# Kernel tuning notes

Measured on AMD Instinct MI355X. Metric: run time of the kernel, lower is better.

The kernel has to match this reference:

```python
import jax, jax.numpy as jnp
import numpy as np

N_PILLARS_X = 512
N_PILLARS_Y = 512
IN_FEATURES = 6
OUT_FEATURES = 64
N_POINTS = 2_000_000
BN_EPS = 1e-5


def setup_inputs() -> dict:
    key = jax.random.key(0)
    k_x, k_idx, k_w, k_b, k_g, k_bt = jax.random.split(key, 6)
    x = jax.random.normal(k_x, (N_POINTS, IN_FEATURES), dtype=jnp.float32)
    indices = jax.random.randint(k_idx, (N_POINTS, 2), 0, N_PILLARS_X, dtype=jnp.int64)
    # Linear params (torch default init scale ~ 1/sqrt(fan_in))
    bound = 1.0 / np.sqrt(IN_FEATURES)
    W = jax.random.uniform(k_w, (OUT_FEATURES, IN_FEATURES), minval=-bound, maxval=bound, dtype=jnp.float32)
    b = jax.random.uniform(k_b, (OUT_FEATURES,), minval=-bound, maxval=bound, dtype=jnp.float32)
    # BatchNorm affine params (torch init: gamma=1, beta=0; perturb gamma slightly)
    gamma = jnp.ones((OUT_FEATURES,), dtype=jnp.float32)
    beta = jnp.zeros((OUT_FEATURES,), dtype=jnp.float32)
    return {"x": x, "indices": indices, "W": W, "b": b, "gamma": gamma, "beta": beta}


def reference(x, indices, W, b, gamma, beta):
    # Linear: (N, 6) @ (6, 64) + b -> (N, 64)
    h = x @ W.T + b
    # BatchNorm1d (training mode: batch statistics, biased variance)
    mean = jnp.mean(h, axis=0)
    var = jnp.mean(jnp.square(h - mean), axis=0)
    h = gamma * (h - mean) * jax.lax.rsqrt(var + BN_EPS) + beta
    h = jax.nn.relu(h)
    # Scatter-add each point's feature vector into its (x_idx, y_idx) pillar cell
    grid = jnp.zeros((N_PILLARS_X, N_PILLARS_Y, OUT_FEATURES), dtype=h.dtype)
    grid = grid.at[indices[:, 0], indices[:, 1]].add(h)
    return grid
```

## Files before the change

### kernel.cpp

```cpp
#include <hip/hip_runtime.h>
#include <hip/hip_fp16.h>


constexpr int NPTS   = 2000000;
constexpr int NBUCK  = 2048;
constexpr int CPB    = 128;
constexpr int NBLK   = 256;
constexpr int CHUNK  = 7813;
constexpr float EPS  = 1e-5f;

constexpr int WS_WPH    = 0;
constexpr int WS_BP     = 192;
constexpr int WS_STARTS = 256;
constexpr int WS_HIST   = 2560;
constexpr int WS_BASES  = WS_HIST + NBLK * NBUCK;
constexpr int WS_BSTATS = WS_BASES + NBLK * NBUCK;
constexpr int WS_SORTED = WS_BSTATS + NBLK * 32;

typedef _Float16 h2v __attribute__((ext_vector_type(2)));

__device__ __forceinline__ float dot2u(unsigned int a, unsigned int b, float c) {
    union { unsigned int u; h2v h; } ca, cb;
    ca.u = a; cb.u = b;
    return __builtin_amdgcn_fdot2(ca.h, cb.h, c, false);
}

__device__ __forceinline__ float wave_sum64(float v) {
#pragma unroll
    for (int off = 32; off > 0; off >>= 1) v += __shfl_down(v, off, 64);
    return v;
}

__global__ __launch_bounds__(1024) void hist_kernel(const int2* __restrict__ idx,
                                                    int* __restrict__ hist) {
    __shared__ int lh[NBUCK];
    for (int i = threadIdx.x; i < NBUCK; i += 1024) lh[i] = 0;
    __syncthreads();
    const int beg = blockIdx.x * CHUNK;
    const int end = min(NPTS, beg + CHUNK);
    for (int p = beg + threadIdx.x; p < end; p += 1024) {
        const int2 ij = idx[p];
        atomicAdd(&lh[(ij.x << 2) | (ij.y >> 7)], 1);
    }
    __syncthreads();
    int* out = hist + blockIdx.x * NBUCK;
    for (int i = threadIdx.x; i < NBUCK; i += 1024) out[i] = lh[i];
}

__global__ __launch_bounds__(64) void colscan_kernel(const int* __restrict__ hist,
                                                     int* __restrict__ bases,
                                                     int* __restrict__ starts) {
    const int b = blockIdx.x * 64 + threadIdx.x;
    int run = 0;
    for (int blk = 0; blk < NBLK; ++blk) {
        bases[blk * NBUCK + b] = run;
        run += hist[blk * NBUCK + b];
    }
    starts[b] = run;
}

__global__ __launch_bounds__(1024) void scan_kernel(int* __restrict__ starts) {
    __shared__ int wsum[16];
    const int t = threadIdx.x, lane = t & 63, wv = t >> 6;
    const int v0 = starts[2 * t], v1 = starts[2 * t + 1];
    const int v = v0 + v1;
    int incl = v;
#pragma unroll
    for (int d = 1; d < 64; d <<= 1) {
        int u = __shfl_up(incl, d, 64);
        if (lane >= d) incl += u;
    }
    if (lane == 63) wsum[wv] = incl;
    __syncthreads();
    int pre = 0;
#pragma unroll
    for (int w = 0; w < 16; ++w) {
        int sv = wsum[w];
        if (w < wv) pre += sv;
    }
    const int excl = pre + incl - v;
    starts[2 * t] = excl;
    starts[2 * t + 1] = excl + v0;
    if (t == 1023) starts[NBUCK] = excl + v;
}

__global__ __launch_bounds__(1024) void scatter_kernel(const float* __restrict__ x,
                                                       const int2* __restrict__ idx,
                                                       const int* __restrict__ starts,
                                                       const int* __restrict__ bases,
                                                       uint4* __restrict__ sorted4,
                                                       float* __restrict__ bstats) {
    __shared__ int lbase[NBUCK];
    __shared__ int lcur[NBUCK];
    __shared__ float lstats[16][27];
    const int blk = blockIdx.x;
    for (int i = threadIdx.x; i < NBUCK; i += 1024) {
        lbase[i] = starts[i] + bases[blk * NBUCK + i];
        lcur[i] = 0;
    }
    __syncthreads();

    float acc[27];
#pragma unroll
    for (int i = 0; i < 27; ++i) acc[i] = 0.f;

    const int beg = blk * CHUNK;
    const int end = min(NPTS, beg + CHUNK);
    for (int p = beg + threadIdx.x; p < end; p += 1024) {
        const int2 ij = idx[p];
        const float2* xp = (const float2*)(x + (size_t)p * 6);
        const float2 a = xp[0], bq = xp[1], cq = xp[2];
        float v[6] = {a.x, a.y, bq.x, bq.y, cq.x, cq.y};
        int c = 6;
#pragma unroll
        for (int k = 0; k < 6; ++k) {
            acc[k] += v[k];
#pragma unroll
            for (int l = k; l < 6; ++l) { acc[c] += v[k] * v[l]; ++c; }
        }
        __half2 h0 = __floats2half2_rn(a.x, a.y);
        __half2 h1 = __floats2half2_rn(bq.x, bq.y);
        __half2 h2 = __floats2half2_rn(cq.x, cq.y);
        const int b = (ij.x << 2) | (ij.y >> 7);
        const int rank = atomicAdd(&lcur[b], 1);
        uint4 r;
        r.x = *(const unsigned int*)&h0;
        r.y = *(const unsigned int*)&h1;
        r.z = *(const unsigned int*)&h2;
        r.w = (unsigned int)(ij.y & 127);
        sorted4[lbase[b] + rank] = r;
    }

    const int lane = threadIdx.x & 63, wv = threadIdx.x >> 6;
#pragma unroll
    for (int i = 0; i < 27; ++i) {
        const float s = wave_sum64(acc[i]);
        if (lane == 0) lstats[wv][i] = s;
    }
    __syncthreads();
    if (threadIdx.x < 27) {
        float s = 0.f;
        for (int w = 0; w < 16; ++w) s += lstats[w][threadIdx.x];
        bstats[blk * 32 + threadIdx.x] = s;
    }
}

__global__ __launch_bounds__(64) void bnfold_kernel(const float* __restrict__ bstats,
                                                    const float* __restrict__ W,
                                                    const float* __restrict__ b,
                                                    const float* __restrict__ gamma,
                                                    const float* __restrict__ beta,
                                                    float* __restrict__ ws) {
    __shared__ float s27[27];
    __shared__ float m[6], C[36];
    const int t = threadIdx.x;
    if (t < 27) {
        float s = 0.f;
        for (int blk = 0; blk < NBLK; ++blk) s += bstats[blk * 32 + t];
        s27[t] = s;
    }
    __syncthreads();
    if (t == 0) {
        const float invN = 1.0f / (float)NPTS;
        float mm[6];
        for (int k = 0; k < 6; ++k) { mm[k] = s27[k] * invN; m[k] = mm[k]; }
        int c = 6;
        for (int k = 0; k < 6; ++k)
            for (int l = k; l < 6; ++l) {
                const float cov = s27[c] * invN - mm[k] * mm[l];
                ++c;
                C[k * 6 + l] = cov;
                C[l * 6 + k] = cov;
            }
    }
    __syncthreads();
    float w[6];
#pragma unroll
    for (int k = 0; k < 6; ++k) w[k] = W[t * 6 + k];
    float mh = b[t];
#pragma unroll
    for (int k = 0; k < 6; ++k) mh += w[k] * m[k];
    float var = 0.f;
#pragma unroll
    for (int k = 0; k < 6; ++k)
#pragma unroll
        for (int l = 0; l < 6; ++l) var += w[k] * w[l] * C[k * 6 + l];
    const float s = gamma[t] * rsqrtf(var + EPS);
    float wp[6];
#pragma unroll
    for (int k = 0; k < 6; ++k) wp[k] = w[k] * s;
    unsigned int* wsu = (unsigned int*)ws;
    __half2 p0 = __floats2half2_rn(wp[0], wp[1]);
    __half2 p1 = __floats2half2_rn(wp[2], wp[3]);
    __half2 p2 = __floats2half2_rn(wp[4], wp[5]);
    wsu[WS_WPH + t * 3 + 0] = *(const unsigned int*)&p0;
    wsu[WS_WPH + t * 3 + 1] = *(const unsigned int*)&p1;
    wsu[WS_WPH + t * 3 + 2] = *(const unsigned int*)&p2;
    ws[WS_BP + t] = beta[t] + s * (b[t] - mh);
}

constexpr int CAP = 1152;
constexpr int ACCT = 256;
constexpr int RPT  = (CAP + ACCT - 1) / ACCT;

__global__ __launch_bounds__(ACCT, 8) void accum_kernel(const uint4* __restrict__ sorted4,
                                                        const int* __restrict__ starts,
                                                        const float* __restrict__ wsf,
                                                        float* __restrict__ grid) {
    __shared__ uint4 recs[CAP];
    __shared__ int lhist[CPB];
    __shared__ int cstart[CPB + 1];
    const int t = threadIdx.x, lane = t & 63, wv = t >> 6;

    const int s = starts[blockIdx.x];
    const int e = starts[blockIdx.x + 1];
    const int n = min(e - s, CAP);

    for (int i = t; i < CPB; i += ACCT) lhist[i] = 0;

    const unsigned int* wsu = (const unsigned int*)wsf;
    const unsigned int wp0 = wsu[WS_WPH + lane * 3 + 0];
    const unsigned int wp1 = wsu[WS_WPH + lane * 3 + 1];
    const unsigned int wp2 = wsu[WS_WPH + lane * 3 + 2];
    const float bb = wsf[WS_BP + lane];
    __syncthreads();

    uint4 rr[RPT];
    int rkk[RPT];
#pragma unroll
    for (int u = 0; u < RPT; ++u) {
        const int i = t + u * ACCT;
        rkk[u] = -1;
        if (i < n) {
            rr[u] = sorted4[s + i];
            rkk[u] = atomicAdd(&lhist[(int)rr[u].w], 1);
        }
    }
    __syncthreads();

    if (wv == 0) {
        const int v0 = lhist[2 * lane], v1 = lhist[2 * lane + 1];
        const int v = v0 + v1;
        int incl = v;
#pragma unroll
        for (int d = 1; d < 64; d <<= 1) {
            int u = __shfl_up(incl, d, 64);
            if (lane >= d) incl += u;
        }
        const int excl = incl - v;
        cstart[2 * lane] = excl;
        cstart[2 * lane + 1] = excl + v0;
        if (lane == 63) cstart[CPB] = incl;
    }
    __syncthreads();

#pragma unroll
    for (int u = 0; u < RPT; ++u)
        if (rkk[u] >= 0) recs[cstart[(int)rr[u].w] + rkk[u]] = rr[u];
    __syncthreads();

    float* gbase = grid + (size_t)blockIdx.x * (CPB * 64);
    for (int c = wv; c < CPB; c += 4) {
        const int cs = __builtin_amdgcn_readfirstlane(cstart[c]);
        const int ce = __builtin_amdgcn_readfirstlane(cstart[c + 1]);
        float acc0 = 0.f, acc1 = 0.f;
        int p = cs;
        for (; p + 1 < ce; p += 2) {
            const uint4 ra = recs[p];
            const uint4 rb = recs[p + 1];
            const float h0 = dot2u(ra.x, wp0, dot2u(ra.y, wp1, dot2u(ra.z, wp2, bb)));
            const float h1 = dot2u(rb.x, wp0, dot2u(rb.y, wp1, dot2u(rb.z, wp2, bb)));
            acc0 += fmaxf(h0, 0.f);
            acc1 += fmaxf(h1, 0.f);
        }
        if (p < ce) {
            const uint4 ra = recs[p];
            acc0 += fmaxf(dot2u(ra.x, wp0, dot2u(ra.y, wp1, dot2u(ra.z, wp2, bb))), 0.f);
        }
        gbase[c * 64 + lane] = acc0 + acc1;
    }

    if (e - s > CAP) {
        __syncthreads();
        for (int base = s + CAP + wv * 64; base < e; base += 4 * 64) {
            const int m = min(64, e - base);
            uint4 rec = make_uint4(0u, 0u, 0u, 0u);
            if (lane < m) rec = sorted4[base + lane];
            for (int pt = 0; pt < m; ++pt) {
                const unsigned int c  = __builtin_amdgcn_readlane(rec.w, pt);
                const unsigned int x0 = __builtin_amdgcn_readlane(rec.x, pt);
                const unsigned int x1 = __builtin_amdgcn_readlane(rec.y, pt);
                const unsigned int x2 = __builtin_amdgcn_readlane(rec.z, pt);
                const float h = dot2u(x0, wp0, dot2u(x1, wp1, dot2u(x2, wp2, bb)));
                unsafeAtomicAdd(&gbase[c * 64 + lane], fmaxf(h, 0.f));
            }
        }
    }
}

extern "C" void kernel_launch(void* const* d_in, const int* in_sizes, int n_in,
                              void* d_out, int out_size, void* d_ws, size_t ws_size,
                              hipStream_t stream) {
    const float* x       = (const float*)d_in[0];
    const int2*  indices = (const int2*)d_in[1];
    const float* W       = (const float*)d_in[2];
    const float* b       = (const float*)d_in[3];
    const float* gamma   = (const float*)d_in[4];
    const float* beta    = (const float*)d_in[5];
    float* out = (float*)d_out;
    float* wsf = (float*)d_ws;
    int*   wsi = (int*)d_ws;

    int*   hist    = wsi + WS_HIST;
    int*   bases   = wsi + WS_BASES;
    int*   starts  = wsi + WS_STARTS;
    uint4* sorted4 = (uint4*)(wsi + WS_SORTED);
    float* bstats  = wsf + WS_BSTATS;

    hist_kernel<<<NBLK, 1024, 0, stream>>>(indices, hist);
    colscan_kernel<<<NBUCK / 64, 64, 0, stream>>>(hist, bases, starts);
    scan_kernel<<<1, 1024, 0, stream>>>(starts);
    scatter_kernel<<<NBLK, 1024, 0, stream>>>(x, indices, starts, bases, sorted4, bstats);
    bnfold_kernel<<<1, 64, 0, stream>>>(bstats, W, b, gamma, beta, wsf);
    accum_kernel<<<NBUCK, ACCT, 0, stream>>>(sorted4, starts, wsf, out);
}
```

Measured before the change: 229.6 us.

## Parallelize column scan into segmented passes with 16-bit histograms and double blocks

```diff
diff --git a/kernel.cpp b/kernel.cpp
--- a/kernel.cpp
+++ b/kernel.cpp
@@ -5,17 +5,21 @@
 constexpr int NPTS   = 2000000;
 constexpr int NBUCK  = 2048;
 constexpr int CPB    = 128;
-constexpr int NBLK   = 256;
-constexpr int CHUNK  = 7813;
+constexpr int NBLK   = 512;
+constexpr int CHUNK  = (NPTS + NBLK - 1) / NBLK;
+constexpr int NSEG   = 8;
+constexpr int SEGLEN = NBLK / NSEG;
 constexpr float EPS  = 1e-5f;
 
 constexpr int WS_WPH    = 0;
 constexpr int WS_BP     = 192;
 constexpr int WS_STARTS = 256;
-constexpr int WS_HIST   = 2560;
-constexpr int WS_BASES  = WS_HIST + NBLK * NBUCK;
-constexpr int WS_BSTATS = WS_BASES + NBLK * NBUCK;
-constexpr int WS_SORTED = WS_BSTATS + NBLK * 32;
+constexpr int WS_SEGT   = 2560;
+constexpr int WS_SEGB   = WS_SEGT + NSEG * NBUCK;
+constexpr int WS_BSTATS = WS_SEGB + NSEG * NBUCK;
+constexpr int WS_HIST16 = WS_BSTATS + NBLK * 32;
+constexpr int WS_BASE16 = WS_HIST16 + NBLK * NBUCK / 2;
+constexpr int WS_SORTED = WS_BASE16 + NBLK * NBUCK / 2;
 
 typedef _Float16 h2v __attribute__((ext_vector_type(2)));
 
@@ -32,7 +36,7 @@
 }
 
 __global__ __launch_bounds__(1024) void hist_kernel(const int2* __restrict__ idx,
-                                                    int* __restrict__ hist) {
+                                                    unsigned int* __restrict__ hist16) {
     __shared__ int lh[NBUCK];
     for (int i = threadIdx.x; i < NBUCK; i += 1024) lh[i] = 0;
     __syncthreads();
@@ -43,20 +47,32 @@
         atomicAdd(&lh[(ij.x << 2) | (ij.y >> 7)], 1);
     }
     __syncthreads();
-    int* out = hist + blockIdx.x * NBUCK;
-    for (int i = threadIdx.x; i < NBUCK; i += 1024) out[i] = lh[i];
-}
-
-__global__ __launch_bounds__(64) void colscan_kernel(const int* __restrict__ hist,
-                                                     int* __restrict__ bases,
-                                                     int* __restrict__ starts) {
-    const int b = blockIdx.x * 64 + threadIdx.x;
+    unsigned int* out = hist16 + blockIdx.x * (NBUCK / 2);
+    for (int i = threadIdx.x; i < NBUCK / 2; i += 1024)
+        out[i] = (unsigned int)lh[2 * i] | ((unsigned int)lh[2 * i + 1] << 16);
+}
+
+__global__ __launch_bounds__(256) void colscan_a(const unsigned short* __restrict__ hist16,
+                                                 int* __restrict__ segtot) {
+    const int gid = blockIdx.x * 256 + threadIdx.x;
+    const int col = gid & (NBUCK - 1), seg = gid >> 11;
+    int s = 0;
+#pragma unroll 8
+    for (int j = 0; j < SEGLEN; ++j) s += hist16[(seg * SEGLEN + j) * NBUCK + col];
+    segtot[seg * NBUCK + col] = s;
+}
+
+__global__ __launch_bounds__(256) void colscan_b(const int* __restrict__ segtot,
+                                                 int* __restrict__ segbase,
+                                                 int* __restrict__ starts) {
+    const int col = blockIdx.x * 256 + threadIdx.x;
     int run = 0;
-    for (int blk = 0; blk < NBLK; ++blk) {
-        bases[blk * NBUCK + b] = run;
-        run += hist[blk * NBUCK + b];
-    }
-    starts[b] = run;
+#pragma unroll
+    for (int sgi = 0; sgi < NSEG; ++sgi) {
+        segbase[sgi * NBUCK + col] = run;
+        run += segtot[sgi * NBUCK + col];
+    }
+    starts[col] = run;
 }
 
 __global__ __launch_bounds__(1024) void scan_kernel(int* __restrict__ starts) {
@@ -84,10 +100,24 @@
     if (t == 1023) starts[NBUCK] = excl + v;
 }
 
+__global__ __launch_bounds__(256) void colscan_c(const unsigned short* __restrict__ hist16,
+                                                 const int* __restrict__ segbase,
+                                                 unsigned short* __restrict__ bases16) {
+    const int gid = blockIdx.x * 256 + threadIdx.x;
+    const int col = gid & (NBUCK - 1), seg = gid >> 11;
+    int run = segbase[seg * NBUCK + col];
+#pragma unroll 8
+    for (int j = 0; j < SEGLEN; ++j) {
+        const int blk = seg * SEGLEN + j;
+        bases16[blk * NBUCK + col] = (unsigned short)run;
+        run += hist16[blk * NBUCK + col];
+    }
+}
+
 __global__ __launch_bounds__(1024) void scatter_kernel(const float* __restrict__ x,
                                                        const int2* __restrict__ idx,
                                                        const int* __restrict__ starts,
-                                                       const int* __restrict__ bases,
+                                                       const unsigned short* __restrict__ bases16,
                                                        uint4* __restrict__ sorted4,
                                                        float* __restrict__ bstats) {
     __shared__ int lbase[NBUCK];
@@ -95,7 +125,7 @@
     __shared__ float lstats[16][27];
     const int blk = blockIdx.x;
     for (int i = threadIdx.x; i < NBUCK; i += 1024) {
-        lbase[i] = starts[i] + bases[blk * NBUCK + i];
+        lbase[i] = starts[i] + (int)bases16[blk * NBUCK + i];
         lcur[i] = 0;
     }
     __syncthreads();
@@ -138,25 +168,36 @@
         if (lane == 0) lstats[wv][i] = s;
     }
     __syncthreads();
-    if (threadIdx.x < 27) {
+    if (threadIdx.x < 32) {
         float s = 0.f;
-        for (int w = 0; w < 16; ++w) s += lstats[w][threadIdx.x];
+        if (threadIdx.x < 27)
+            for (int w = 0; w < 16; ++w) s += lstats[w][threadIdx.x];
         bstats[blk * 32 + threadIdx.x] = s;
     }
 }
 
-__global__ __launch_bounds__(64) void bnfold_kernel(const float* __restrict__ bstats,
-                                                    const float* __restrict__ W,
-                                                    const float* __restrict__ b,
-                                                    const float* __restrict__ gamma,
-                                                    const float* __restrict__ beta,
-                                                    float* __restrict__ ws) {
+__global__ __launch_bounds__(1024) void bnfold_kernel(const float* __restrict__ bstats,
+                                                      const float* __restrict__ W,
+                                                      const float* __restrict__ b,
+                                                      const float* __restrict__ gamma,
+                                                      const float* __restrict__ beta,
+                                                      float* __restrict__ ws) {
+    __shared__ float lred[32][33];
     __shared__ float s27[27];
     __shared__ float m[6], C[36];
     const int t = threadIdx.x;
+    {
+        const int s = t & 31, seg = t >> 5;
+        float a = 0.f;
+#pragma unroll 4
+        for (int j = 0; j < NBLK / 32; ++j) a += bstats[(seg * (NBLK / 32) + j) * 32 + s];
+        lred[seg][s] = a;
+    }
+    __syncthreads();
     if (t < 27) {
         float s = 0.f;
-        for (int blk = 0; blk < NBLK; ++blk) s += bstats[blk * 32 + t];
+#pragma unroll
+        for (int g = 0; g < 32; ++g) s += lred[g][t];
         s27[t] = s;
     }
     __syncthreads();
@@ -174,29 +215,31 @@
             }
     }
     __syncthreads();
-    float w[6];
-#pragma unroll
-    for (int k = 0; k < 6; ++k) w[k] = W[t * 6 + k];
-    float mh = b[t];
-#pragma unroll
-    for (int k = 0; k < 6; ++k) mh += w[k] * m[k];
-    float var = 0.f;
-#pragma unroll
-    for (int k = 0; k < 6; ++k)
-#pragma unroll
-        for (int l = 0; l < 6; ++l) var += w[k] * w[l] * C[k * 6 + l];
-    const float s = gamma[t] * rsqrtf(var + EPS);
-    float wp[6];
-#pragma unroll
-    for (int k = 0; k < 6; ++k) wp[k] = w[k] * s;
-    unsigned int* wsu = (unsigned int*)ws;
-    __half2 p0 = __floats2half2_rn(wp[0], wp[1]);
-    __half2 p1 = __floats2half2_rn(wp[2], wp[3]);
-    __half2 p2 = __floats2half2_rn(wp[4], wp[5]);
-    wsu[WS_WPH + t * 3 + 0] = *(const unsigned int*)&p0;
-    wsu[WS_WPH + t * 3 + 1] = *(const unsigned int*)&p1;
-    wsu[WS_WPH + t * 3 + 2] = *(const unsigned int*)&p2;
-    ws[WS_BP + t] = beta[t] + s * (b[t] - mh);
+    if (t < 64) {
+        float w[6];
+#pragma unroll
+        for (int k = 0; k < 6; ++k) w[k] = W[t * 6 + k];
+        float mh = b[t];
+#pragma unroll
+        for (int k = 0; k < 6; ++k) mh += w[k] * m[k];
+        float var = 0.f;
+#pragma unroll
+        for (int k = 0; k < 6; ++k)
+#pragma unroll
+            for (int l = 0; l < 6; ++l) var += w[k] * w[l] * C[k * 6 + l];
+        const float s = gamma[t] * rsqrtf(var + EPS);
+        float wp[6];
+#pragma unroll
+        for (int k = 0; k < 6; ++k) wp[k] = w[k] * s;
+        unsigned int* wsu = (unsigned int*)ws;
+        __half2 p0 = __floats2half2_rn(wp[0], wp[1]);
+        __half2 p1 = __floats2half2_rn(wp[2], wp[3]);
+        __half2 p2 = __floats2half2_rn(wp[4], wp[5]);
+        wsu[WS_WPH + t * 3 + 0] = *(const unsigned int*)&p0;
+        wsu[WS_WPH + t * 3 + 1] = *(const unsigned int*)&p1;
+        wsu[WS_WPH + t * 3 + 2] = *(const unsigned int*)&p2;
+        ws[WS_BP + t] = beta[t] + s * (b[t] - mh);
+    }
 }
 
 constexpr int CAP = 1152;
@@ -311,16 +354,21 @@
     float* wsf = (float*)d_ws;
     int*   wsi = (int*)d_ws;
 
-    int*   hist    = wsi + WS_HIST;
-    int*   bases   = wsi + WS_BASES;
+    unsigned int*   hist16u = (unsigned int*)(wsi + WS_HIST16);
+    unsigned short* hist16  = (unsigned short*)(wsi + WS_HIST16);
+    unsigned short* bases16 = (unsigned short*)(wsi + WS_BASE16);
+    int*   segtot  = wsi + WS_SEGT;
+    int*   segbase = wsi + WS_SEGB;
     int*   starts  = wsi + WS_STARTS;
     uint4* sorted4 = (uint4*)(wsi + WS_SORTED);
     float* bstats  = wsf + WS_BSTATS;
 
-    hist_kernel<<<NBLK, 1024, 0, stream>>>(indices, hist);
-    colscan_kernel<<<NBUCK / 64, 64, 0, stream>>>(hist, bases, starts);
+    hist_kernel<<<NBLK, 1024, 0, stream>>>(indices, hist16u);
+    colscan_a<<<NSEG * NBUCK / 256, 256, 0, stream>>>(hist16, segtot);
+    colscan_b<<<NBUCK / 256, 256, 0, stream>>>(segtot, segbase, starts);
     scan_kernel<<<1, 1024, 0, stream>>>(starts);
-    scatter_kernel<<<NBLK, 1024, 0, stream>>>(x, indices, starts, bases, sorted4, bstats);
-    bnfold_kernel<<<1, 64, 0, stream>>>(bstats, W, b, gamma, beta, wsf);
+    colscan_c<<<NSEG * NBUCK / 256, 256, 0, stream>>>(hist16, segbase, bases16);
+    scatter_kernel<<<NBLK, 1024, 0, stream>>>(x, indices, starts, bases16, sorted4, bstats);
+    bnfold_kernel<<<1, 1024, 0, stream>>>(bstats, W, b, gamma, beta, wsf);
     accum_kernel<<<NBUCK, ACCT, 0, stream>>>(sorted4, starts, wsf, out);
 }
```

New measurement: 216.9 us. -5.5%, faster.

## Replace histogram-scan sort with fixed-capacity bucket slots plus overflow list

Applied to the files above, without the earlier changes.

```diff
diff --git a/kernel.cpp b/kernel.cpp
--- a/kernel.cpp
+++ b/kernel.cpp
@@ -5,17 +5,22 @@
 constexpr int NPTS   = 2000000;
 constexpr int NBUCK  = 2048;
 constexpr int CPB    = 128;
-constexpr int NBLK   = 256;
-constexpr int CHUNK  = 7813;
+constexpr int NBLK   = 512;
+constexpr int CHUNK  = (NPTS + NBLK - 1) / NBLK;
 constexpr float EPS  = 1e-5f;
+
+constexpr int CAPR = 1148;
+constexpr int OCAP = 4096;
+constexpr int ACCT = 256;
+constexpr int RPT  = (CAPR + ACCT - 1) / ACCT;
 
 constexpr int WS_WPH    = 0;
 constexpr int WS_BP     = 192;
-constexpr int WS_STARTS = 256;
-constexpr int WS_HIST   = 2560;
-constexpr int WS_BASES  = WS_HIST + NBLK * NBUCK;
-constexpr int WS_BSTATS = WS_BASES + NBLK * NBUCK;
-constexpr int WS_SORTED = WS_BSTATS + NBLK * 32;
+constexpr int WS_BCUR   = 256;
+constexpr int WS_OCNT   = WS_BCUR + NBUCK * 16;
+constexpr int WS_BSTATS = WS_OCNT + 16;
+constexpr int WS_OLIST  = WS_BSTATS + NBLK * 32;
+constexpr int WS_SORTED = WS_OLIST + OCAP * 4;
 
 typedef _Float16 h2v __attribute__((ext_vector_type(2)));
 
@@ -31,74 +36,15 @@
     return v;
 }
 
-__global__ __launch_bounds__(1024) void hist_kernel(const int2* __restrict__ idx,
-                                                    int* __restrict__ hist) {
-    __shared__ int lh[NBUCK];
-    for (int i = threadIdx.x; i < NBUCK; i += 1024) lh[i] = 0;
-    __syncthreads();
-    const int beg = blockIdx.x * CHUNK;
-    const int end = min(NPTS, beg + CHUNK);
-    for (int p = beg + threadIdx.x; p < end; p += 1024) {
-        const int2 ij = idx[p];
-        atomicAdd(&lh[(ij.x << 2) | (ij.y >> 7)], 1);
-    }
-    __syncthreads();
-    int* out = hist + blockIdx.x * NBUCK;
-    for (int i = threadIdx.x; i < NBUCK; i += 1024) out[i] = lh[i];
-}
-
-__global__ __launch_bounds__(64) void colscan_kernel(const int* __restrict__ hist,
-                                                     int* __restrict__ bases,
-                                                     int* __restrict__ starts) {
-    const int b = blockIdx.x * 64 + threadIdx.x;
-    int run = 0;
-    for (int blk = 0; blk < NBLK; ++blk) {
-        bases[blk * NBUCK + b] = run;
-        run += hist[blk * NBUCK + b];
-    }
-    starts[b] = run;
-}
-
-__global__ __launch_bounds__(1024) void scan_kernel(int* __restrict__ starts) {
-    __shared__ int wsum[16];
-    const int t = threadIdx.x, lane = t & 63, wv = t >> 6;
-    const int v0 = starts[2 * t], v1 = starts[2 * t + 1];
-    const int v = v0 + v1;
-    int incl = v;
-#pragma unroll
-    for (int d = 1; d < 64; d <<= 1) {
-        int u = __shfl_up(incl, d, 64);
-        if (lane >= d) incl += u;
-    }
-    if (lane == 63) wsum[wv] = incl;
-    __syncthreads();
-    int pre = 0;
-#pragma unroll
-    for (int w = 0; w < 16; ++w) {
-        int sv = wsum[w];
-        if (w < wv) pre += sv;
-    }
-    const int excl = pre + incl - v;
-    starts[2 * t] = excl;
-    starts[2 * t + 1] = excl + v0;
-    if (t == 1023) starts[NBUCK] = excl + v;
-}
-
 __global__ __launch_bounds__(1024) void scatter_kernel(const float* __restrict__ x,
                                                        const int2* __restrict__ idx,
-                                                       const int* __restrict__ starts,
-                                                       const int* __restrict__ bases,
+                                                       int* __restrict__ wsi,
                                                        uint4* __restrict__ sorted4,
+                                                       uint4* __restrict__ olist,
                                                        float* __restrict__ bstats) {
-    __shared__ int lbase[NBUCK];
-    __shared__ int lcur[NBUCK];
     __shared__ float lstats[16][27];
+    int* bcur = wsi + WS_BCUR;
     const int blk = blockIdx.x;
-    for (int i = threadIdx.x; i < NBUCK; i += 1024) {
-        lbase[i] = starts[i] + bases[blk * NBUCK + i];
-        lcur[i] = 0;
-    }
-    __syncthreads();
 
     float acc[27];
 #pragma unroll
@@ -121,14 +67,20 @@
         __half2 h0 = __floats2half2_rn(a.x, a.y);
         __half2 h1 = __floats2half2_rn(bq.x, bq.y);
         __half2 h2 = __floats2half2_rn(cq.x, cq.y);
-        const int b = (ij.x << 2) | (ij.y >> 7);
-        const int rank = atomicAdd(&lcur[b], 1);
+        const int cell = (ij.x << 9) | ij.y;
+        const int bk = cell >> 7;
+        const int slot = atomicAdd(&bcur[bk * 16], 1);
         uint4 r;
         r.x = *(const unsigned int*)&h0;
         r.y = *(const unsigned int*)&h1;
         r.z = *(const unsigned int*)&h2;
-        r.w = (unsigned int)(ij.y & 127);
-        sorted4[lbase[b] + rank] = r;
+        if (slot < CAPR) {
+            r.w = (unsigned int)(cell & 127);
+            sorted4[(size_t)bk * CAPR + slot] = r;
+        } else {
+            const int os = atomicAdd(wsi + WS_OCNT, 1);
+            if (os < OCAP) { r.w = (unsigned int)cell; olist[os] = r; }
+        }
     }
 
     const int lane = threadIdx.x & 63, wv = threadIdx.x >> 6;
@@ -138,25 +90,36 @@
         if (lane == 0) lstats[wv][i] = s;
     }
     __syncthreads();
-    if (threadIdx.x < 27) {
+    if (threadIdx.x < 32) {
         float s = 0.f;
-        for (int w = 0; w < 16; ++w) s += lstats[w][threadIdx.x];
+        if (threadIdx.x < 27)
+            for (int w = 0; w < 16; ++w) s += lstats[w][threadIdx.x];
         bstats[blk * 32 + threadIdx.x] = s;
     }
 }
 
-__global__ __launch_bounds__(64) void bnfold_kernel(const float* __restrict__ bstats,
-                                                    const float* __restrict__ W,
-                                                    const float* __restrict__ b,
-                                                    const float* __restrict__ gamma,
-                                                    const float* __restrict__ beta,
-                                                    float* __restrict__ ws) {
+__global__ __launch_bounds__(1024) void bnfold_kernel(const float* __restrict__ bstats,
+                                                      const float* __restrict__ W,
+                                                      const float* __restrict__ b,
+                                                      const float* __restrict__ gamma,
+                                                      const float* __restrict__ beta,
+                                                      float* __restrict__ ws) {
+    __shared__ float lred[32][33];
     __shared__ float s27[27];
     __shared__ float m[6], C[36];
     const int t = threadIdx.x;
+    {
+        const int s = t & 31, seg = t >> 5;
+        float a = 0.f;
+#pragma unroll 4
+        for (int j = 0; j < NBLK / 32; ++j) a += bstats[(seg * (NBLK / 32) + j) * 32 + s];
+        lred[seg][s] = a;
+    }
+    __syncthreads();
     if (t < 27) {
         float s = 0.f;
-        for (int blk = 0; blk < NBLK; ++blk) s += bstats[blk * 32 + t];
+#pragma unroll
+        for (int g = 0; g < 32; ++g) s += lred[g][t];
         s27[t] = s;
     }
     __syncthreads();
@@ -174,47 +137,44 @@
             }
     }
     __syncthreads();
-    float w[6];
-#pragma unroll
-    for (int k = 0; k < 6; ++k) w[k] = W[t * 6 + k];
-    float mh = b[t];
-#pragma unroll
-    for (int k = 0; k < 6; ++k) mh += w[k] * m[k];
-    float var = 0.f;
-#pragma unroll
-    for (int k = 0; k < 6; ++k)
-#pragma unroll
-        for (int l = 0; l < 6; ++l) var += w[k] * w[l] * C[k * 6 + l];
-    const float s = gamma[t] * rsqrtf(var + EPS);
-    float wp[6];
-#pragma unroll
-    for (int k = 0; k < 6; ++k) wp[k] = w[k] * s;
-    unsigned int* wsu = (unsigned int*)ws;
-    __half2 p0 = __floats2half2_rn(wp[0], wp[1]);
-    __half2 p1 = __floats2half2_rn(wp[2], wp[3]);
-    __half2 p2 = __floats2half2_rn(wp[4], wp[5]);
-    wsu[WS_WPH + t * 3 + 0] = *(const unsigned int*)&p0;
-    wsu[WS_WPH + t * 3 + 1] = *(const unsigned int*)&p1;
-    wsu[WS_WPH + t * 3 + 2] = *(const unsigned int*)&p2;
-    ws[WS_BP + t] = beta[t] + s * (b[t] - mh);
-}
-
-constexpr int CAP = 1152;
-constexpr int ACCT = 256;
-constexpr int RPT  = (CAP + ACCT - 1) / ACCT;
+    if (t < 64) {
+        float w[6];
+#pragma unroll
+        for (int k = 0; k < 6; ++k) w[k] = W[t * 6 + k];
+        float mh = b[t];
+#pragma unroll
+        for (int k = 0; k < 6; ++k) mh += w[k] * m[k];
+        float var = 0.f;
+#pragma unroll
+        for (int k = 0; k < 6; ++k)
+#pragma unroll
+            for (int l = 0; l < 6; ++l) var += w[k] * w[l] * C[k * 6 + l];
+        const float s = gamma[t] * rsqrtf(var + EPS);
+        float wp[6];
+#pragma unroll
+        for (int k = 0; k < 6; ++k) wp[k] = w[k] * s;
+        unsigned int* wsu = (unsigned int*)ws;
+        __half2 p0 = __floats2half2_rn(wp[0], wp[1]);
+        __half2 p1 = __floats2half2_rn(wp[2], wp[3]);
+        __half2 p2 = __floats2half2_rn(wp[4], wp[5]);
+        wsu[WS_WPH + t * 3 + 0] = *(const unsigned int*)&p0;
+        wsu[WS_WPH + t * 3 + 1] = *(const unsigned int*)&p1;
+        wsu[WS_WPH + t * 3 + 2] = *(const unsigned int*)&p2;
+        ws[WS_BP + t] = beta[t] + s * (b[t] - mh);
+    }
+}
 
 __global__ __launch_bounds__(ACCT, 8) void accum_kernel(const uint4* __restrict__ sorted4,
-                                                        const int* __restrict__ starts,
+                                                        const int* __restrict__ wsi,
                                                         const float* __restrict__ wsf,
+                                                        const uint4* __restrict__ olist,
                                                         float* __restrict__ grid) {
-    __shared__ uint4 recs[CAP];
+    __shared__ uint4 recs[CAPR];
     __shared__ int lhist[CPB];
     __shared__ int cstart[CPB + 1];
     const int t = threadIdx.x, lane = t & 63, wv = t >> 6;
-
-    const int s = starts[blockIdx.x];
-    const int e = starts[blockIdx.x + 1];
-    const int n = min(e - s, CAP);
+    const int b = blockIdx.x;
+    const int n = min(wsi[WS_BCUR + b * 16], CAPR);
 
     for (int i = t; i < CPB; i += ACCT) lhist[i] = 0;
 
@@ -225,6 +185,7 @@
     const float bb = wsf[WS_BP + lane];
     __syncthreads();
 
+    const uint4* src = sorted4 + (size_t)b * CAPR;
     uint4 rr[RPT];
     int rkk[RPT];
 #pragma unroll
@@ -232,7 +193,7 @@
         const int i = t + u * ACCT;
         rkk[u] = -1;
         if (i < n) {
-            rr[u] = sorted4[s + i];
+            rr[u] = src[i];
             rkk[u] = atomicAdd(&lhist[(int)rr[u].w], 1);
         }
     }
@@ -259,40 +220,53 @@
         if (rkk[u] >= 0) recs[cstart[(int)rr[u].w] + rkk[u]] = rr[u];
     __syncthreads();
 
-    float* gbase = grid + (size_t)blockIdx.x * (CPB * 64);
-    for (int c = wv; c < CPB; c += 4) {
-        const int cs = __builtin_amdgcn_readfirstlane(cstart[c]);
-        const int ce = __builtin_amdgcn_readfirstlane(cstart[c + 1]);
-        float acc0 = 0.f, acc1 = 0.f;
-        int p = cs;
-        for (; p + 1 < ce; p += 2) {
-            const uint4 ra = recs[p];
-            const uint4 rb = recs[p + 1];
-            const float h0 = dot2u(ra.x, wp0, dot2u(ra.y, wp1, dot2u(ra.z, wp2, bb)));
-            const float h1 = dot2u(rb.x, wp0, dot2u(rb.y, wp1, dot2u(rb.z, wp2, bb)));
-            acc0 += fmaxf(h0, 0.f);
-            acc1 += fmaxf(h1, 0.f);
-        }
-        if (p < ce) {
-            const uint4 ra = recs[p];
-            acc0 += fmaxf(dot2u(ra.x, wp0, dot2u(ra.y, wp1, dot2u(ra.z, wp2, bb))), 0.f);
-        }
-        gbase[c * 64 + lane] = acc0 + acc1;
-    }
-
-    if (e - s > CAP) {
+    float* gbase = grid + (size_t)b * (CPB * 64);
+    const int c0 = wv * 32, climit = c0 + 32;
+    int c = c0;
+    int ce = __builtin_amdgcn_readfirstlane(cstart[c0 + 1]);
+    const int wbeg = __builtin_amdgcn_readfirstlane(cstart[c0]);
+    const int wend = __builtin_amdgcn_readfirstlane(cstart[climit]);
+    float acc = 0.f;
+
+    auto flush = [&](int pnext) {
+        while (c < climit && ce == pnext) {
+            gbase[c * 64 + lane] = acc;
+            acc = 0.f;
+            ++c;
+            if (c < climit) ce = __builtin_amdgcn_readfirstlane(cstart[c + 1]);
+        }
+    };
+    flush(wbeg);
+    int p = wbeg;
+    for (; p + 4 <= wend; p += 4) {
+        const uint4 r0 = recs[p];
+        const uint4 r1 = recs[p + 1];
+        const uint4 r2 = recs[p + 2];
+        const uint4 r3 = recs[p + 3];
+        const float h0 = dot2u(r0.x, wp0, dot2u(r0.y, wp1, dot2u(r0.z, wp2, bb)));
+        const float h1 = dot2u(r1.x, wp0, dot2u(r1.y, wp1, dot2u(r1.z, wp2, bb)));
+        const float h2 = dot2u(r2.x, wp0, dot2u(r2.y, wp1, dot2u(r2.z, wp2, bb)));
+        const float h3 = dot2u(r3.x, wp0, dot2u(r3.y, wp1, dot2u(r3.z, wp2, bb)));
+        acc += fmaxf(h0, 0.f); flush(p + 1);
+        acc += fmaxf(h1, 0.f); flush(p + 2);
+        acc += fmaxf(h2, 0.f); flush(p + 3);
+        acc += fmaxf(h3, 0.f); flush(p + 4);
+    }
+    for (; p < wend; ++p) {
+        const uint4 r0 = recs[p];
+        acc += fmaxf(dot2u(r0.x, wp0, dot2u(r0.y, wp1, dot2u(r0.z, wp2, bb))), 0.f);
+        flush(p + 1);
+    }
+
+    const int ocn = min(wsi[WS_OCNT], OCAP);
+    if (ocn > 0) {
         __syncthreads();
-        for (int base = s + CAP + wv * 64; base < e; base += 4 * 64) {
-            const int m = min(64, e - base);
-            uint4 rec = make_uint4(0u, 0u, 0u, 0u);
-            if (lane < m) rec = sorted4[base + lane];
-            for (int pt = 0; pt < m; ++pt) {
-                const unsigned int c  = __builtin_amdgcn_readlane(rec.w, pt);
-                const unsigned int x0 = __builtin_amdgcn_readlane(rec.x, pt);
-                const unsigned int x1 = __builtin_amdgcn_readlane(rec.y, pt);
-                const unsigned int x2 = __builtin_amdgcn_readlane(rec.z, pt);
-                const float h = dot2u(x0, wp0, dot2u(x1, wp1, dot2u(x2, wp2, bb)));
-                unsafeAtomicAdd(&gbase[c * 64 + lane], fmaxf(h, 0.f));
+        for (int i = wv; i < ocn; i += 4) {
+            const uint4 r = olist[i];
+            const int cell = (int)r.w;
+            if ((cell >> 7) == b) {
+                const float h = dot2u(r.x, wp0, dot2u(r.y, wp1, dot2u(r.z, wp2, bb)));
+                unsafeAtomicAdd(&gbase[(cell & 127) * 64 + lane], fmaxf(h, 0.f));
             }
         }
     }
@@ -311,16 +285,12 @@
     float* wsf = (float*)d_ws;
     int*   wsi = (int*)d_ws;
 
-    int*   hist    = wsi + WS_HIST;
-    int*   bases   = wsi + WS_BASES;
-    int*   starts  = wsi + WS_STARTS;
     uint4* sorted4 = (uint4*)(wsi + WS_SORTED);
+    uint4* olist   = (uint4*)(wsi + WS_OLIST);
     float* bstats  = wsf + WS_BSTATS;
 
-    hist_kernel<<<NBLK, 1024, 0, stream>>>(indices, hist);
-    colscan_kernel<<<NBUCK / 64, 64, 0, stream>>>(hist, bases, starts);
-    scan_kernel<<<1, 1024, 0, stream>>>(starts);
-    scatter_kernel<<<NBLK, 1024, 0, stream>>>(x, indices, starts, bases, sorted4, bstats);
-    bnfold_kernel<<<1, 64, 0, stream>>>(bstats, W, b, gamma, beta, wsf);
-    accum_kernel<<<NBUCK, ACCT, 0, stream>>>(sorted4, starts, wsf, out);
-}
+    hipMemsetAsync(wsi + WS_BCUR, 0, (size_t)(WS_BSTATS - WS_BCUR) * sizeof(int), stream);
+    scatter_kernel<<<NBLK, 1024, 0, stream>>>(x, indices, wsi, sorted4, olist, bstats);
+    bnfold_kernel<<<1, 1024, 0, stream>>>(bstats, W, b, gamma, beta, wsf);
+    accum_kernel<<<NBUCK, ACCT, 0, stream>>>(sorted4, wsi, wsf, olist, out);
+}
```

Measured after the change: 285.3 us. 24.2% more time.

## Fuse histogram, scan and scatter into block-local LDS sort with per-chunk regions

Applied to the files above, without the earlier changes.

```diff
diff --git a/kernel.cpp b/kernel.cpp
--- a/kernel.cpp
+++ b/kernel.cpp
@@ -5,17 +5,15 @@
 constexpr int NPTS   = 2000000;
 constexpr int NBUCK  = 2048;
 constexpr int CPB    = 128;
-constexpr int NBLK   = 256;
-constexpr int CHUNK  = 7813;
+constexpr int NBLK   = 512;
+constexpr int CHUNK  = (NPTS + NBLK - 1) / NBLK;
 constexpr float EPS  = 1e-5f;
 
 constexpr int WS_WPH    = 0;
 constexpr int WS_BP     = 192;
-constexpr int WS_STARTS = 256;
-constexpr int WS_HIST   = 2560;
-constexpr int WS_BASES  = WS_HIST + NBLK * NBUCK;
-constexpr int WS_BSTATS = WS_BASES + NBLK * NBUCK;
-constexpr int WS_SORTED = WS_BSTATS + NBLK * 32;
+constexpr int WS_BSTATS = 256;
+constexpr int WS_OFFT   = WS_BSTATS + NBLK * 32;
+constexpr int WS_REG    = WS_OFFT + (NBUCK + 1) * NBLK / 2;
 
 typedef _Float16 h2v __attribute__((ext_vector_type(2)));
 
@@ -31,82 +29,59 @@
     return v;
 }
 
-__global__ __launch_bounds__(1024) void hist_kernel(const int2* __restrict__ idx,
-                                                    int* __restrict__ hist) {
+__global__ __launch_bounds__(1024) void sort_kernel(const float* __restrict__ x,
+                                                    const int2* __restrict__ idx,
+                                                    unsigned short* __restrict__ offt,
+                                                    uint4* __restrict__ regions,
+                                                    float* __restrict__ bstats) {
+    __shared__ uint4 recs[CHUNK];
     __shared__ int lh[NBUCK];
-    for (int i = threadIdx.x; i < NBUCK; i += 1024) lh[i] = 0;
-    __syncthreads();
-    const int beg = blockIdx.x * CHUNK;
-    const int end = min(NPTS, beg + CHUNK);
-    for (int p = beg + threadIdx.x; p < end; p += 1024) {
+    __shared__ int wsum[16];
+    __shared__ float lstats[16][27];
+    const int t = threadIdx.x, lane = t & 63, wv = t >> 6;
+    const int blk = blockIdx.x;
+    const int ch  = ((blk & 7) << 6) | (blk >> 3);
+    const int beg = ch * CHUNK, end = min(NPTS, beg + CHUNK), cnt = end - beg;
+
+    for (int i = t; i < NBUCK; i += 1024) lh[i] = 0;
+    __syncthreads();
+
+    for (int p = beg + t; p < end; p += 1024) {
         const int2 ij = idx[p];
         atomicAdd(&lh[(ij.x << 2) | (ij.y >> 7)], 1);
     }
     __syncthreads();
-    int* out = hist + blockIdx.x * NBUCK;
-    for (int i = threadIdx.x; i < NBUCK; i += 1024) out[i] = lh[i];
-}
-
-__global__ __launch_bounds__(64) void colscan_kernel(const int* __restrict__ hist,
-                                                     int* __restrict__ bases,
-                                                     int* __restrict__ starts) {
-    const int b = blockIdx.x * 64 + threadIdx.x;
-    int run = 0;
-    for (int blk = 0; blk < NBLK; ++blk) {
-        bases[blk * NBUCK + b] = run;
-        run += hist[blk * NBUCK + b];
-    }
-    starts[b] = run;
-}
-
-__global__ __launch_bounds__(1024) void scan_kernel(int* __restrict__ starts) {
-    __shared__ int wsum[16];
-    const int t = threadIdx.x, lane = t & 63, wv = t >> 6;
-    const int v0 = starts[2 * t], v1 = starts[2 * t + 1];
-    const int v = v0 + v1;
-    int incl = v;
-#pragma unroll
-    for (int d = 1; d < 64; d <<= 1) {
-        int u = __shfl_up(incl, d, 64);
-        if (lane >= d) incl += u;
-    }
-    if (lane == 63) wsum[wv] = incl;
-    __syncthreads();
-    int pre = 0;
-#pragma unroll
-    for (int w = 0; w < 16; ++w) {
-        int sv = wsum[w];
-        if (w < wv) pre += sv;
-    }
-    const int excl = pre + incl - v;
-    starts[2 * t] = excl;
-    starts[2 * t + 1] = excl + v0;
-    if (t == 1023) starts[NBUCK] = excl + v;
-}
-
-__global__ __launch_bounds__(1024) void scatter_kernel(const float* __restrict__ x,
-                                                       const int2* __restrict__ idx,
-                                                       const int* __restrict__ starts,
-                                                       const int* __restrict__ bases,
-                                                       uint4* __restrict__ sorted4,
-                                                       float* __restrict__ bstats) {
-    __shared__ int lbase[NBUCK];
-    __shared__ int lcur[NBUCK];
-    __shared__ float lstats[16][27];
-    const int blk = blockIdx.x;
-    for (int i = threadIdx.x; i < NBUCK; i += 1024) {
-        lbase[i] = starts[i] + bases[blk * NBUCK + i];
-        lcur[i] = 0;
+
+    {
+        const int v0 = lh[2 * t], v1 = lh[2 * t + 1];
+        const int v = v0 + v1;
+        int incl = v;
+#pragma unroll
+        for (int d = 1; d < 64; d <<= 1) {
+            int u = __shfl_up(incl, d, 64);
+            if (lane >= d) incl += u;
+        }
+        if (lane == 63) wsum[wv] = incl;
+        __syncthreads();
+        int pre = 0;
+#pragma unroll
+        for (int w = 0; w < 16; ++w) {
+            int sv = wsum[w];
+            if (w < wv) pre += sv;
+        }
+        const int excl = pre + incl - v;
+        offt[(2 * t) * NBLK + ch]     = (unsigned short)excl;
+        offt[(2 * t + 1) * NBLK + ch] = (unsigned short)(excl + v0);
+        if (t == 1023) offt[NBUCK * NBLK + ch] = (unsigned short)(excl + v);
+        lh[2 * t] = excl;
+        lh[2 * t + 1] = excl + v0;
     }
     __syncthreads();
 
     float acc[27];
 #pragma unroll
     for (int i = 0; i < 27; ++i) acc[i] = 0.f;
-
-    const int beg = blk * CHUNK;
-    const int end = min(NPTS, beg + CHUNK);
-    for (int p = beg + threadIdx.x; p < end; p += 1024) {
+    for (int p = beg + t; p < end; p += 1024) {
         const int2 ij = idx[p];
         const float2* xp = (const float2*)(x + (size_t)p * 6);
         const float2 a = xp[0], bq = xp[1], cq = xp[2];
@@ -122,41 +97,55 @@
         __half2 h1 = __floats2half2_rn(bq.x, bq.y);
         __half2 h2 = __floats2half2_rn(cq.x, cq.y);
         const int b = (ij.x << 2) | (ij.y >> 7);
-        const int rank = atomicAdd(&lcur[b], 1);
+        const int dst = atomicAdd(&lh[b], 1);
         uint4 r;
         r.x = *(const unsigned int*)&h0;
         r.y = *(const unsigned int*)&h1;
         r.z = *(const unsigned int*)&h2;
         r.w = (unsigned int)(ij.y & 127);
-        sorted4[lbase[b] + rank] = r;
-    }
-
-    const int lane = threadIdx.x & 63, wv = threadIdx.x >> 6;
+        recs[dst] = r;
+    }
+    __syncthreads();
+
+    uint4* reg = regions + (size_t)ch * CHUNK;
+    for (int i = t; i < cnt; i += 1024) reg[i] = recs[i];
+
 #pragma unroll
     for (int i = 0; i < 27; ++i) {
         const float s = wave_sum64(acc[i]);
         if (lane == 0) lstats[wv][i] = s;
     }
     __syncthreads();
-    if (threadIdx.x < 27) {
+    if (t < 32) {
         float s = 0.f;
-        for (int w = 0; w < 16; ++w) s += lstats[w][threadIdx.x];
-        bstats[blk * 32 + threadIdx.x] = s;
-    }
-}
-
-__global__ __launch_bounds__(64) void bnfold_kernel(const float* __restrict__ bstats,
-                                                    const float* __restrict__ W,
-                                                    const float* __restrict__ b,
-                                                    const float* __restrict__ gamma,
-                                                    const float* __restrict__ beta,
-                                                    float* __restrict__ ws) {
+        if (t < 27)
+            for (int w = 0; w < 16; ++w) s += lstats[w][t];
+        bstats[ch * 32 + t] = s;
+    }
+}
+
+__global__ __launch_bounds__(1024) void bnfold_kernel(const float* __restrict__ bstats,
+                                                      const float* __restrict__ W,
+                                                      const float* __restrict__ b,
+                                                      const float* __restrict__ gamma,
+                                                      const float* __restrict__ beta,
+                                                      float* __restrict__ ws) {
+    __shared__ float lred[32][33];
     __shared__ float s27[27];
     __shared__ float m[6], C[36];
     const int t = threadIdx.x;
+    {
+        const int s = t & 31, seg = t >> 5;
+        float a = 0.f;
+#pragma unroll 4
+        for (int j = 0; j < NBLK / 32; ++j) a += bstats[(seg * (NBLK / 32) + j) * 32 + s];
+        lred[seg][s] = a;
+    }
+    __syncthreads();
     if (t < 27) {
         float s = 0.f;
-        for (int blk = 0; blk < NBLK; ++blk) s += bstats[blk * 32 + t];
+#pragma unroll
+        for (int g = 0; g < 32; ++g) s += lred[g][t];
         s27[t] = s;
     }
     __syncthreads();
@@ -174,66 +163,112 @@
             }
     }
     __syncthreads();
-    float w[6];
-#pragma unroll
-    for (int k = 0; k < 6; ++k) w[k] = W[t * 6 + k];
-    float mh = b[t];
-#pragma unroll
-    for (int k = 0; k < 6; ++k) mh += w[k] * m[k];
-    float var = 0.f;
-#pragma unroll
-    for (int k = 0; k < 6; ++k)
-#pragma unroll
-        for (int l = 0; l < 6; ++l) var += w[k] * w[l] * C[k * 6 + l];
-    const float s = gamma[t] * rsqrtf(var + EPS);
-    float wp[6];
-#pragma unroll
-    for (int k = 0; k < 6; ++k) wp[k] = w[k] * s;
-    unsigned int* wsu = (unsigned int*)ws;
-    __half2 p0 = __floats2half2_rn(wp[0], wp[1]);
-    __half2 p1 = __floats2half2_rn(wp[2], wp[3]);
-    __half2 p2 = __floats2half2_rn(wp[4], wp[5]);
-    wsu[WS_WPH + t * 3 + 0] = *(const unsigned int*)&p0;
-    wsu[WS_WPH + t * 3 + 1] = *(const unsigned int*)&p1;
-    wsu[WS_WPH + t * 3 + 2] = *(const unsigned int*)&p2;
-    ws[WS_BP + t] = beta[t] + s * (b[t] - mh);
-}
-
-constexpr int CAP = 1152;
-constexpr int ACCT = 256;
-constexpr int RPT  = (CAP + ACCT - 1) / ACCT;
-
-__global__ __launch_bounds__(ACCT, 8) void accum_kernel(const uint4* __restrict__ sorted4,
-                                                        const int* __restrict__ starts,
+    if (t < 64) {
+        float w[6];
+#pragma unroll
+        for (int k = 0; k < 6; ++k) w[k] = W[t * 6 + k];
+        float mh = b[t];
+#pragma unroll
+        for (int k = 0; k < 6; ++k) mh += w[k] * m[k];
+        float var = 0.f;
+#pragma unroll
+        for (int k = 0; k < 6; ++k)
+#pragma unroll
+            for (int l = 0; l < 6; ++l) var += w[k] * w[l] * C[k * 6 + l];
+        const float s = gamma[t] * rsqrtf(var + EPS);
+        float wp[6];
+#pragma unroll
+        for (int k = 0; k < 6; ++k) wp[k] = w[k] * s;
+        unsigned int* wsu = (unsigned int*)ws;
+        __half2 p0 = __floats2half2_rn(wp[0], wp[1]);
+        __half2 p1 = __floats2half2_rn(wp[2], wp[3]);
+        __half2 p2 = __floats2half2_rn(wp[4], wp[5]);
+        wsu[WS_WPH + t * 3 + 0] = *(const unsigned int*)&p0;
+        wsu[WS_WPH + t * 3 + 1] = *(const unsigned int*)&p1;
+        wsu[WS_WPH + t * 3 + 2] = *(const unsigned int*)&p2;
+        ws[WS_BP + t] = beta[t] + s * (b[t] - mh);
+    }
+}
+
+constexpr int CAP   = 1216;
+constexpr int OVCAP = 64;
+constexpr int ACCT  = 256;
+constexpr int RPT   = (CAP + ACCT - 1) / ACCT;
+
+__global__ __launch_bounds__(ACCT, 8) void accum_kernel(const uint4* __restrict__ regions,
+                                                        const unsigned int* __restrict__ offt32,
                                                         const float* __restrict__ wsf,
                                                         float* __restrict__ grid) {
     __shared__ uint4 recs[CAP];
+    __shared__ uint4 ovf[OVCAP];
     __shared__ int lhist[CPB];
     __shared__ int cstart[CPB + 1];
+    __shared__ int wsum4[4];
+    __shared__ int ntot, novf;
     const int t = threadIdx.x, lane = t & 63, wv = t >> 6;
-
-    const int s = starts[blockIdx.x];
-    const int e = starts[blockIdx.x + 1];
-    const int n = min(e - s, CAP);
+    const int b = blockIdx.x;
 
     for (int i = t; i < CPB; i += ACCT) lhist[i] = 0;
+    if (t == 0) novf = 0;
 
     const unsigned int* wsu = (const unsigned int*)wsf;
     const unsigned int wp0 = wsu[WS_WPH + lane * 3 + 0];
     const unsigned int wp1 = wsu[WS_WPH + lane * 3 + 1];
     const unsigned int wp2 = wsu[WS_WPH + lane * 3 + 2];
     const float bb = wsf[WS_BP + lane];
-    __syncthreads();
-
-    uint4 rr[RPT];
-    int rkk[RPT];
+
+    const unsigned int A = offt32[b * (NBLK / 2) + t];
+    const unsigned int B = offt32[(b + 1) * (NBLK / 2) + t];
+    const int o0 = (int)(A & 0xffffu), o1 = (int)(A >> 16);
+    const int l0 = (int)(B & 0xffffu) - o0, l1 = (int)(B >> 16) - o1;
+    const int tot = l0 + l1;
+    int incl = tot;
+#pragma unroll
+    for (int d = 1; d < 64; d <<= 1) {
+        int u = __shfl_up(incl, d, 64);
+        if (lane >= d) incl += u;
+    }
+    if (lane == 63) wsum4[wv] = incl;
+    __syncthreads();
+    int pre = 0;
+#pragma unroll
+    for (int w = 0; w < 4; ++w) {
+        int sv = wsum4[w];
+        if (w < wv) pre += sv;
+    }
+    const int base0 = pre + incl - tot;
+    const int base1 = base0 + l0;
+    if (t == ACCT - 1) ntot = base1 + l1;
+
+    {
+        const uint4* s0 = regions + (size_t)(2 * t) * CHUNK + o0;
+        for (int k = 0; k < l0; ++k) {
+            const uint4 r = s0[k];
+            const int dst = base0 + k;
+            if (dst < CAP) recs[dst] = r;
+            else { int sl = atomicAdd(&novf, 1); if (sl < OVCAP) ovf[sl] = r; }
+        }
+        const uint4* s1 = regions + (size_t)(2 * t + 1) * CHUNK + o1;
+        for (int k = 0; k < l1; ++k) {
+            const uint4 r = s1[k];
+            const int dst = base1 + k;
+            if (dst < CAP) recs[dst] = r;
+            else { int sl = atomicAdd(&novf, 1); if (sl < OVCAP) ovf[sl] = r; }
+        }
+    }
+    __syncthreads();
+    const int nn = min(ntot, CAP);
+    const int ovn = min(novf, OVCAP);
+
+    uint4 rv[RPT];
+    int rk[RPT];
 #pragma unroll
     for (int u = 0; u < RPT; ++u) {
         const int i = t + u * ACCT;
-        rkk[u] = -1;
-        if (i < n) {
-            rr[u] = sorted4[s + i];
-            rkk[u] = atomicAdd(&lhist[(int)rr[u].w], 1);
+        rk[u] = -1;
+        if (i < nn) {
+            rv[u] = recs[i];
+            rk[u] = atomicAdd(&lhist[(int)rv[u].w], 1);
         }
     }
     __syncthreads();
@@ -241,25 +276,25 @@
     if (wv == 0) {
         const int v0 = lhist[2 * lane], v1 = lhist[2 * lane + 1];
         const int v = v0 + v1;
-        int incl = v;
+        int incl2 = v;
 #pragma unroll
         for (int d = 1; d < 64; d <<= 1) {
-            int u = __shfl_up(incl, d, 64);
-            if (lane >= d) incl += u;
-        }
-        const int excl = incl - v;
+            int u = __shfl_up(incl2, d, 64);
+            if (lane >= d) incl2 += u;
+        }
+        const int excl = incl2 - v;
         cstart[2 * lane] = excl;
         cstart[2 * lane + 1] = excl + v0;
-        if (lane == 63) cstart[CPB] = incl;
+        if (lane == 63) cstart[CPB] = incl2;
     }
     __syncthreads();
 
 #pragma unroll
     for (int u = 0; u < RPT; ++u)
-        if (rkk[u] >= 0) recs[cstart[(int)rr[u].w] + rkk[u]] = rr[u];
-    __syncthreads();
-
-    float* gbase = grid + (size_t)blockIdx.x * (CPB * 64);
+        if (rk[u] >= 0) recs[cstart[(int)rv[u].w] + rk[u]] = rv[u];
+    __syncthreads();
+
+    float* gbase = grid + (size_t)b * (CPB * 64);
     for (int c = wv; c < CPB; c += 4) {
         const int cs = __builtin_amdgcn_readfirstlane(cstart[c]);
         const int ce = __builtin_amdgcn_readfirstlane(cstart[c + 1]);
@@ -280,20 +315,13 @@
         gbase[c * 64 + lane] = acc0 + acc1;
     }
 
-    if (e - s > CAP) {
+    if (ovn > 0) {
         __syncthreads();
-        for (int base = s + CAP + wv * 64; base < e; base += 4 * 64) {
-            const int m = min(64, e - base);
-            uint4 rec = make_uint4(0u, 0u, 0u, 0u);
-            if (lane < m) rec = sorted4[base + lane];
-            for (int pt = 0; pt < m; ++pt) {
-                const unsigned int c  = __builtin_amdgcn_readlane(rec.w, pt);
-                const unsigned int x0 = __builtin_amdgcn_readlane(rec.x, pt);
-                const unsigned int x1 = __builtin_amdgcn_readlane(rec.y, pt);
-                const unsigned int x2 = __builtin_amdgcn_readlane(rec.z, pt);
-                const float h = dot2u(x0, wp0, dot2u(x1, wp1, dot2u(x2, wp2, bb)));
-                unsafeAtomicAdd(&gbase[c * 64 + lane], fmaxf(h, 0.f));
-            }
+        for (int i = wv; i < ovn; i += 4) {
+            const uint4 r = ovf[i];
+            const int c = (int)r.w;
+            const float h = dot2u(r.x, wp0, dot2u(r.y, wp1, dot2u(r.z, wp2, bb)));
+            unsafeAtomicAdd(&gbase[c * 64 + lane], fmaxf(h, 0.f));
         }
     }
 }
@@ -311,16 +339,12 @@
     float* wsf = (float*)d_ws;
     int*   wsi = (int*)d_ws;
 
-    int*   hist    = wsi + WS_HIST;
-    int*   bases   = wsi + WS_BASES;
-    int*   starts  = wsi + WS_STARTS;
-    uint4* sorted4 = (uint4*)(wsi + WS_SORTED);
+    unsigned short* offt   = (unsigned short*)(wsi + WS_OFFT);
+    unsigned int*   offt32 = (unsigned int*)(wsi + WS_OFFT);
+    uint4* regions = (uint4*)(wsi + WS_REG);
     float* bstats  = wsf + WS_BSTATS;
 
-    hist_kernel<<<NBLK, 1024, 0, stream>>>(indices, hist);
-    colscan_kernel<<<NBUCK / 64, 64, 0, stream>>>(hist, bases, starts);
-    scan_kernel<<<1, 1024, 0, stream>>>(starts);
-    scatter_kernel<<<NBLK, 1024, 0, stream>>>(x, indices, starts, bases, sorted4, bstats);
-    bnfold_kernel<<<1, 64, 0, stream>>>(bstats, W, b, gamma, beta, wsf);
-    accum_kernel<<<NBUCK, ACCT, 0, stream>>>(sorted4, starts, wsf, out);
-}
+    sort_kernel<<<NBLK, 1024, 0, stream>>>(x, indices, offt, regions, bstats);
+    bnfold_kernel<<<1, 1024, 0, stream>>>(bstats, W, b, gamma, beta, wsf);
+    accum_kernel<<<NBUCK, ACCT, 0, stream>>>(regions, offt32, wsf, out);
+}
```

Result: faster. 206.2 us (-10.2%).
